# Kernel tuning notes

Measured on AMD Instinct MI355X. Metric: run time of the kernel, lower is better.

Reference implementation:

```python
import jax, jax.numpy as jnp
import numpy as np

KS = 3          # deformable kernel size
PAD = 1         # zero padding
N = KS * KS     # sampling points per pixel
INC = 64
OUTC = 64


def _conv(x, w, stride, pad, groups):
    return jax.lax.conv_general_dilated(
        x, w, (stride, stride), ((pad, pad), (pad, pad)),
        feature_group_count=groups,
        dimension_numbers=('NCHW', 'OIHW', 'NCHW'))


def setup_inputs() -> dict:
    key = jax.random.key(0)
    k = jax.random.split(key, 5)
    b, h, w = 4, 128, 128
    x = jax.random.normal(k[0], (b, INC, h, w), jnp.float32)
    # SeparableConv2d params (bias=False throughout in source)
    p_dw = jax.random.normal(k[1], (INC, 1, 3, 3), jnp.float32) * 0.1     # p_conv depthwise 3x3 pad1
    p_pw = jax.random.normal(k[2], (2 * N, INC, 1, 1), jnp.float32) * 0.1  # p_conv pointwise -> 2N offsets
    c_dw = jax.random.normal(k[3], (INC, 1, KS, KS), jnp.float32) * 0.1    # conv depthwise k=ks stride=ks
    c_pw = jax.random.normal(k[4], (OUTC, INC, 1, 1), jnp.float32) * 0.1   # conv pointwise
    return {'x': x, 'p_dw': p_dw, 'p_pw': p_pw, 'c_dw': c_dw, 'c_pw': c_pw}


def reference(x, p_dw, p_pw, c_dw, c_pw):
    b, c, h, w = x.shape
    offset = _conv(_conv(x, p_dw, 1, 1, INC), p_pw, 1, 0, 1)   # [b, 2N, h, w]
    xp = jnp.pad(x, ((0, 0), (0, 0), (PAD, PAD), (PAD, PAD)))  # zero_padding
    Hp, Wp = h + 2 * PAD, w + 2 * PAD
    # p_n: kernel-relative offsets (row-major over ks x ks, 'ij' meshgrid)
    r = jnp.arange(-(KS - 1) // 2, (KS - 1) // 2 + 1, dtype=jnp.float32)
    pnx, pny = jnp.meshgrid(r, r, indexing='ij')
    p_n = jnp.concatenate([pnx.ravel(), pny.ravel()])[None, :, None, None]  # [1, 2N, 1, 1]
    # p_0: base grid, 1-indexed (accounts for padding), stride=1
    gx = jnp.arange(1, h + 1, dtype=jnp.float32)[None, None, :, None]
    gy = jnp.arange(1, w + 1, dtype=jnp.float32)[None, None, None, :]
    p0 = jnp.concatenate([jnp.broadcast_to(gx, (1, N, h, w)),
                          jnp.broadcast_to(gy, (1, N, h, w))], axis=1)      # [1, 2N, h, w]
    p = (p0 + p_n + offset).transpose(0, 2, 3, 1)                           # [b, h, w, 2N]
    px, py = p[..., :N], p[..., N:]
    fx, fy = jnp.floor(px), jnp.floor(py)
    ltx = jnp.clip(fx, 0, Hp - 1); lty = jnp.clip(fy, 0, Wp - 1)
    rbx = jnp.clip(fx + 1, 0, Hp - 1); rby = jnp.clip(fy + 1, 0, Wp - 1)
    pxc = jnp.clip(px, 0, Hp - 1); pyc = jnp.clip(py, 0, Wp - 1)
    # bilinear weights
    g_lt = (1 + (ltx - pxc)) * (1 + (lty - pyc))
    g_rb = (1 - (rbx - pxc)) * (1 - (rby - pyc))
    g_lb = (1 + (ltx - pxc)) * (1 - (rby - pyc))
    g_rt = (1 - (rbx - pxc)) * (1 + (lty - pyc))
    x_flat = xp.reshape(b, c, Hp * Wp)

    def gather(qx, qy):  # -> [b, c, h, w, N]
        idx = (qx * Wp + qy).astype(jnp.int32).reshape(b, 1, h * w * N)
        return jnp.take_along_axis(x_flat, idx, axis=2).reshape(b, c, h, w, N)

    x_off = (g_lt[:, None] * gather(ltx, lty) + g_rb[:, None] * gather(rbx, rby)
             + g_lb[:, None] * gather(ltx, rby) + g_rt[:, None] * gather(rbx, lty))
    # _reshape_x_offset: [b,c,h,w,N] -> [b,c,h*ks,w*ks]
    x_off = x_off.reshape(b, c, h, w, KS, KS).transpose(0, 1, 2, 4, 3, 5).reshape(b, c, h * KS, w * KS)
    # SeparableConv2d(inc, outc, k=ks, stride=ks)
    return _conv(_conv(x_off, c_dw, KS, 0, INC), c_pw, 1, 0, 1)
```

## Files before the change

kernel.cpp:

```cpp
#include <hip/hip_runtime.h>
#include <hip/hip_fp16.h>

#define Hdim 128
#define Wdim 128
#define Cdim 64
#define HW   (Hdim * Wdim)
#define NPIX (4 * HW)
#define NBLK (NPIX / 64)
#define NXCD 8
#define Hp 130
#define HWp (Hp * Hp)

typedef _Float16 v8h __attribute__((ext_vector_type(8)));
typedef float    v4f __attribute__((ext_vector_type(4)));

__device__ __forceinline__ int xcd_swizzle(int bid, int nblk) {
    return (bid % NXCD) * (nblk / NXCD) + bid / NXCD;
}

__global__ __launch_bounds__(512) void transpose_kernel(
    const float* __restrict__ x,
    __half* __restrict__ xt)
{
    __shared__ float tile[64][65];
    int lane = threadIdx.x & 63;
    int g    = threadIdx.x >> 6;
    int blk  = xcd_swizzle(blockIdx.x, NBLK);
    int pix0 = blk * 64;
    int b    = pix0 >> 14;
    int hw0  = pix0 & (HW - 1);
    int h    = hw0 >> 7;
    int w0   = hw0 & 127;

    {
        int gid = blockIdx.x * 512 + threadIdx.x;
        if (gid < 2064 * 8) {
            int rp  = gid >> 3, sub = gid & 7;
            int img = rp / 516, pos = rp - img * 516;
            int i, j;
            if (pos < 130)      { i = 0;   j = pos; }
            else if (pos < 260) { i = 129; j = pos - 130; }
            else { int p2 = pos - 260; i = 1 + (p2 >> 1); j = (p2 & 1) ? 129 : 0; }
            float4* dst = (float4*)(xt + ((size_t)img * HWp + i * Hp + j) * Cdim);
            dst[sub] = make_float4(0.f, 0.f, 0.f, 0.f);
        }
    }

#pragma unroll
    for (int i = 0; i < 8; ++i) {
        int c = g * 8 + i;
        tile[c][lane] = x[(size_t)(b * Cdim + c) * HW + hw0 + lane];
    }
    __syncthreads();
#pragma unroll
    for (int i = 0; i < 8; ++i) {
        int p = g * 8 + i;
        size_t ppos = ((size_t)b * HWp + (h + 1) * Hp + (w0 + 1 + p)) * Cdim + lane;
        xt[ppos] = (__half)tile[lane][p];
    }
}

__global__ __launch_bounds__(512) void fused_kernel(
    const float* __restrict__ x,
    const float* __restrict__ p_dw,
    const float* __restrict__ p_pw,
    const __half* __restrict__ xt,
    const float* __restrict__ c_dw,
    const float* __restrict__ c_pw,
    float* __restrict__ out)
{
    __shared__ __align__(16) unsigned char smem[26880];
    __shared__ __align__(16) unsigned int geoL[8][320];

    auto part_h = (_Float16 (*)[18][64])smem;
    auto accs_h = (_Float16 (*)[72])smem;
    auto outD   = (float (*)[69])(smem + 9216);

    int lane = threadIdx.x & 63;
    int g    = threadIdx.x >> 6;
    int blk  = xcd_swizzle(blockIdx.x, NBLK);
    int pix0 = blk * 64;
    int pix  = pix0 + lane;
    int w = pix & (Wdim - 1);
    int h = (pix >> 7) & (Hdim - 1);
    int b = pix >> 14;

    int   off9[9];
    float msk9[9];
#pragma unroll
    for (int dh = -1; dh <= 1; ++dh) {
#pragma unroll
        for (int dw = -1; dw <= 1; ++dw) {
            int tap = (dh + 1) * 3 + (dw + 1);
            int hh = h + dh, ww = w + dw;
            bool ok = (hh >= 0) & (hh < Hdim) & (ww >= 0) & (ww < Wdim);
            off9[tap] = ok ? hh * Wdim + ww : 0;
            msk9[tap] = ok ? 1.f : 0.f;
        }
    }

    float t[8];
#pragma unroll
    for (int i = 0; i < 8; ++i) {
        int c = g * 8 + i;
        const float* xb0 = x + (size_t)(b * Cdim + c) * HW;
        float s = 0.f;
#pragma unroll
        for (int tap = 0; tap < 9; ++tap) {
            float v = xb0[off9[tap]] * msk9[tap];
            s += v * p_dw[c * 9 + tap];
        }
        t[i] = s;
    }

#pragma unroll
    for (int j = 0; j < 18; ++j) {
        float s = 0.f;
#pragma unroll
        for (int i = 0; i < 8; ++i)
            s += p_pw[j * Cdim + g * 8 + i] * t[i];
        part_h[g][j][lane] = (_Float16)s;
    }
    __syncthreads();

#pragma unroll
    for (int it = 0; it < 3; ++it) {
        int idx = threadIdx.x + it * 512;
        if (idx < 18 * 64) {
            int j = idx >> 6;
            int p = idx & 63;
            float s = 0.f;
#pragma unroll
            for (int q = 0; q < 8; ++q) s += (float)part_h[q][j][p];
            part_h[0][j][p] = (_Float16)s;
        }
    }
    __syncthreads();

#pragma unroll
    for (int it = 0; it < 2; ++it) {
        int idx = threadIdx.x + it * 512;
        if (idx < 9 * 64) {
            int k = idx >> 6;
            int p = idx & 63;
            int ppix = pix0 + p;
            int pw2 = ppix & (Wdim - 1);
            int ph2 = (ppix >> 7) & (Hdim - 1);

            float px = (float)(ph2 + 1) + (float)(k / 3 - 1) + (float)part_h[0][k][p];
            float py = (float)(pw2 + 1) + (float)(k % 3 - 1) + (float)part_h[0][k + 9][p];

            float fx = floorf(px), fy = floorf(py);
            float ltx = fminf(fmaxf(fx, 0.f), 129.f);
            float lty = fminf(fmaxf(fy, 0.f), 129.f);
            float rbx = fminf(fmaxf(fx + 1.f, 0.f), 129.f);
            float rby = fminf(fmaxf(fy + 1.f, 0.f), 129.f);
            float pxc = fminf(fmaxf(px, 0.f), 129.f);
            float pyc = fminf(fmaxf(py, 0.f), 129.f);

            float glt = (1.f + ltx - pxc) * (1.f + lty - pyc);
            float grb = (1.f - rbx + pxc) * (1.f - rby + pyc);
            float glb = (1.f + ltx - pxc) * (1.f - rby + pyc);
            float grt = (1.f - rbx + pxc) * (1.f + lty - pyc);

            int ix0 = (int)ltx, iy0 = (int)lty, ix1 = (int)rbx, iy1 = (int)rby;

            int base1, base2;
            if (iy1 == iy0 + 1) {
                base1 = ix0 * Hp + iy0;
                base2 = ix1 * Hp + iy0;
            } else {
                glt = glb = grt = grb = 0.f;
                base1 = base2 = 0;
            }

            __half2 wlo = __floats2half2_rn(glt, grt);
            __half2 whi = __floats2half2_rn(glb, grb);
            uint4 pk;
            pk.x = *(const unsigned int*)&wlo;
            pk.y = *(const unsigned int*)&whi;
            pk.z = (unsigned int)base1;
            pk.w = (unsigned int)base2;
            *(uint4*)&geoL[p >> 3][(k * 8 + (p & 7)) * 4] = pk;
        }
    }
    __syncthreads();

    int c2   = lane & 31;
    bool lo  = lane < 32;
    int gu   = __builtin_amdgcn_readfirstlane(g);
    const __half* xb = xt + (size_t)b * HWp * Cdim;

    int gv0, gv1, gv2, gv3, gv4;
    {
        const unsigned int* gb = &geoL[gu][0] + lane;
        gv0 = gb[0];   gv1 = gb[64];  gv2 = gb[128];
        gv3 = gb[192]; gv4 = gb[256];
    }
    float wkx9[9], wky9[9];
#pragma unroll
    for (int k = 0; k < 9; ++k) {
        wkx9[k] = c_dw[(2 * c2) * 9 + k];
        wky9[k] = c_dw[(2 * c2 + 1) * 9 + k];
    }

#define GV(r) ((r)==0?gv0:(r)==1?gv1:(r)==2?gv2:(r)==3?gv3:gv4)
#define RL(f) __builtin_amdgcn_readlane(GV((f) >> 6), (f) & 63)

    float2 acc2[8];
#pragma unroll
    for (int i = 0; i < 8; ++i) acc2[i] = make_float2(0.f, 0.f);

#pragma unroll
    for (int k = 0; k < 9; ++k) {
#pragma unroll
        for (int i = 0; i < 8; ++i) {
            const int f = (k * 8 + i) * 4;
            unsigned int d0 = (unsigned int)RL(f + 0);
            unsigned int d1 = (unsigned int)RL(f + 1);
            int bs1 = RL(f + 2);
            int bs2 = RL(f + 3);
            const unsigned int* p1 = (const unsigned int*)(xb + ((size_t)bs1 << 6));
            const unsigned int* p2 = (const unsigned int*)(xb + ((size_t)bs2 << 6));
            unsigned int v1 = p1[lane];
            unsigned int v2 = p2[lane];
            unsigned int wsu = lo ? d0 : d1;
            __half2 w12 = *(const __half2*)&wsu;
            __half2 v1h = *(const __half2*)&v1;
            __half2 v2h = *(const __half2*)&v2;
            __half2 tt = __hadd2(__hmul2(v1h, __half2half2(__low2half(w12))),
                                 __hmul2(v2h, __half2half2(__high2half(w12))));
            float2 tf = __half22float2(tt);
            acc2[i].x += wkx9[k] * tf.x;
            acc2[i].y += wky9[k] * tf.y;
        }
    }
#undef RL
#undef GV

#pragma unroll
    for (int i = 0; i < 8; ++i) {
        acc2[i].x += __shfl_xor(acc2[i].x, 32);
        acc2[i].y += __shfl_xor(acc2[i].y, 32);
    }
    if (lo) {
#pragma unroll
        for (int i = 0; i < 8; ++i) {
            __half2 hv = __floats2half2_rn(acc2[i].x, acc2[i].y);
            *(__half2*)&accs_h[gu * 8 + i][2 * c2] = hv;
        }
    }
    __syncthreads();

    {
        int pb = gu & 3;
        int ob = gu >> 2;
        int lr = lane & 15;
        int lg = lane >> 4;

        const v8h a0 = *(const v8h*)&accs_h[pb * 16 + lr][lg * 8];
        const v8h a1 = *(const v8h*)&accs_h[pb * 16 + lr][32 + lg * 8];

        v4f d0 = {0.f, 0.f, 0.f, 0.f}, d1 = {0.f, 0.f, 0.f, 0.f};
#pragma unroll
        for (int t2 = 0; t2 < 2; ++t2) {
            int oc = ob * 32 + t2 * 16 + lr;
            const float* wr = c_pw + oc * Cdim + lg * 8;
            v8h b0, b1;
#pragma unroll
            for (int j = 0; j < 8; ++j) {
                b0[j] = (_Float16)wr[j];
                b1[j] = (_Float16)wr[32 + j];
            }
            if (t2 == 0) {
                d0 = __builtin_amdgcn_mfma_f32_16x16x32_f16(a0, b0, d0, 0, 0, 0);
                d0 = __builtin_amdgcn_mfma_f32_16x16x32_f16(a1, b1, d0, 0, 0, 0);
            } else {
                d1 = __builtin_amdgcn_mfma_f32_16x16x32_f16(a0, b0, d1, 0, 0, 0);
                d1 = __builtin_amdgcn_mfma_f32_16x16x32_f16(a1, b1, d1, 0, 0, 0);
            }
        }

#pragma unroll
        for (int r = 0; r < 4; ++r) {
            outD[pb * 16 + lg * 4 + r][ob * 32 + lr]      = d0[r];
            outD[pb * 16 + lg * 4 + r][ob * 32 + 16 + lr] = d1[r];
        }
    }
    __syncthreads();

    int hw = pix & (HW - 1);
    size_t obase = (size_t)b * Cdim * HW + hw;
#pragma unroll
    for (int i = 0; i < 8; ++i)
        out[obase + (size_t)(gu * 8 + i) * HW] = outD[lane][gu * 8 + i];
}

extern "C" void kernel_launch(void* const* d_in, const int* in_sizes, int n_in,
                              void* d_out, int out_size, void* d_ws, size_t ws_size,
                              hipStream_t stream) {
    const float* x    = (const float*)d_in[0];
    const float* p_dw = (const float*)d_in[1];
    const float* p_pw = (const float*)d_in[2];
    const float* c_dw = (const float*)d_in[3];
    const float* c_pw = (const float*)d_in[4];
    float* out = (float*)d_out;

    __half* xt = (__half*)d_ws;

    transpose_kernel<<<dim3(NBLK), dim3(512), 0, stream>>>(x, xt);
    fused_kernel<<<dim3(NBLK), dim3(512), 0, stream>>>(x, p_dw, p_pw, xt, c_dw, c_pw, out);
}
```

Baseline: 54.52 us.

## Fuse offset partial reduction into geometry pass and accumulate gather in half2

Removes the separate reduction pass over the per-group offset partials and its barrier by summing the eight partials directly where sampling geometry is computed. Precomputes byte offsets (base shifted by 7) so the gather loop does a single add instead of a shift and multiply. Keeps the depthwise weights and accumulators as packed half2 and uses hfma2, replacing the float converts and scalar FMAs. The shuffle reduction is done on packed half2. Accumulating nine taps in fp16 risks extra rounding error compared with the fp32 accumulation it replaces.

```diff
diff --git a/kernel.cpp b/kernel.cpp
--- a/kernel.cpp
+++ b/kernel.cpp
@@ -124,31 +124,25 @@
     __syncthreads();
 
 #pragma unroll
-    for (int it = 0; it < 3; ++it) {
-        int idx = threadIdx.x + it * 512;
-        if (idx < 18 * 64) {
-            int j = idx >> 6;
-            int p = idx & 63;
-            float s = 0.f;
-#pragma unroll
-            for (int q = 0; q < 8; ++q) s += (float)part_h[q][j][p];
-            part_h[0][j][p] = (_Float16)s;
-        }
-    }
-    __syncthreads();
-
-#pragma unroll
     for (int it = 0; it < 2; ++it) {
         int idx = threadIdx.x + it * 512;
         if (idx < 9 * 64) {
             int k = idx >> 6;
             int p = idx & 63;
+
+            float offx = 0.f, offy = 0.f;
+#pragma unroll
+            for (int q = 0; q < 8; ++q) {
+                offx += (float)part_h[q][k][p];
+                offy += (float)part_h[q][k + 9][p];
+            }
+
             int ppix = pix0 + p;
             int pw2 = ppix & (Wdim - 1);
             int ph2 = (ppix >> 7) & (Hdim - 1);
 
-            float px = (float)(ph2 + 1) + (float)(k / 3 - 1) + (float)part_h[0][k][p];
-            float py = (float)(pw2 + 1) + (float)(k % 3 - 1) + (float)part_h[0][k + 9][p];
+            float px = (float)(ph2 + 1) + (float)(k / 3 - 1) + offx;
+            float py = (float)(pw2 + 1) + (float)(k % 3 - 1) + offy;
 
             float fx = floorf(px), fy = floorf(py);
             float ltx = fminf(fmaxf(fx, 0.f), 129.f);
@@ -165,13 +159,13 @@
 
             int ix0 = (int)ltx, iy0 = (int)lty, ix1 = (int)rbx, iy1 = (int)rby;
 
-            int base1, base2;
+            unsigned int bb1, bb2;
             if (iy1 == iy0 + 1) {
-                base1 = ix0 * Hp + iy0;
-                base2 = ix1 * Hp + iy0;
+                bb1 = (unsigned int)(ix0 * Hp + iy0) << 7;
+                bb2 = (unsigned int)(ix1 * Hp + iy0) << 7;
             } else {
                 glt = glb = grt = grb = 0.f;
-                base1 = base2 = 0;
+                bb1 = bb2 = 0;
             }
 
             __half2 wlo = __floats2half2_rn(glt, grt);
@@ -179,8 +173,8 @@
             uint4 pk;
             pk.x = *(const unsigned int*)&wlo;
             pk.y = *(const unsigned int*)&whi;
-            pk.z = (unsigned int)base1;
-            pk.w = (unsigned int)base2;
+            pk.z = bb1;
+            pk.w = bb2;
             *(uint4*)&geoL[p >> 3][(k * 8 + (p & 7)) * 4] = pk;
         }
     }
@@ -189,7 +183,7 @@
     int c2   = lane & 31;
     bool lo  = lane < 32;
     int gu   = __builtin_amdgcn_readfirstlane(g);
-    const __half* xb = xt + (size_t)b * HWp * Cdim;
+    const char* xbB = (const char*)(xt + (size_t)b * HWp * Cdim) + (lane << 2);
 
     int gv0, gv1, gv2, gv3, gv4;
     {
@@ -197,19 +191,18 @@
         gv0 = gb[0];   gv1 = gb[64];  gv2 = gb[128];
         gv3 = gb[192]; gv4 = gb[256];
     }
-    float wkx9[9], wky9[9];
-#pragma unroll
-    for (int k = 0; k < 9; ++k) {
-        wkx9[k] = c_dw[(2 * c2) * 9 + k];
-        wky9[k] = c_dw[(2 * c2 + 1) * 9 + k];
-    }
+    __half2 wk2h[9];
+#pragma unroll
+    for (int k = 0; k < 9; ++k)
+        wk2h[k] = __floats2half2_rn(c_dw[(2 * c2) * 9 + k],
+                                    c_dw[(2 * c2 + 1) * 9 + k]);
 
 #define GV(r) ((r)==0?gv0:(r)==1?gv1:(r)==2?gv2:(r)==3?gv3:gv4)
 #define RL(f) __builtin_amdgcn_readlane(GV((f) >> 6), (f) & 63)
 
-    float2 acc2[8];
-#pragma unroll
-    for (int i = 0; i < 8; ++i) acc2[i] = make_float2(0.f, 0.f);
+    __half2 acch[8];
+#pragma unroll
+    for (int i = 0; i < 8; ++i) acch[i] = __floats2half2_rn(0.f, 0.f);
 
 #pragma unroll
     for (int k = 0; k < 9; ++k) {
@@ -218,21 +211,17 @@
             const int f = (k * 8 + i) * 4;
             unsigned int d0 = (unsigned int)RL(f + 0);
             unsigned int d1 = (unsigned int)RL(f + 1);
-            int bs1 = RL(f + 2);
-            int bs2 = RL(f + 3);
-            const unsigned int* p1 = (const unsigned int*)(xb + ((size_t)bs1 << 6));
-            const unsigned int* p2 = (const unsigned int*)(xb + ((size_t)bs2 << 6));
-            unsigned int v1 = p1[lane];
-            unsigned int v2 = p2[lane];
+            unsigned int bb1 = (unsigned int)RL(f + 2);
+            unsigned int bb2 = (unsigned int)RL(f + 3);
+            unsigned int v1 = *(const unsigned int*)(xbB + bb1);
+            unsigned int v2 = *(const unsigned int*)(xbB + bb2);
             unsigned int wsu = lo ? d0 : d1;
             __half2 w12 = *(const __half2*)&wsu;
             __half2 v1h = *(const __half2*)&v1;
             __half2 v2h = *(const __half2*)&v2;
-            __half2 tt = __hadd2(__hmul2(v1h, __half2half2(__low2half(w12))),
-                                 __hmul2(v2h, __half2half2(__high2half(w12))));
-            float2 tf = __half22float2(tt);
-            acc2[i].x += wkx9[k] * tf.x;
-            acc2[i].y += wky9[k] * tf.y;
+            __half2 tt = __hfma2(v2h, __half2half2(__high2half(w12)),
+                                 __hmul2(v1h, __half2half2(__low2half(w12))));
+            acch[i] = __hfma2(wk2h[k], tt, acch[i]);
         }
     }
 #undef RL
@@ -240,15 +229,14 @@
 
 #pragma unroll
     for (int i = 0; i < 8; ++i) {
-        acc2[i].x += __shfl_xor(acc2[i].x, 32);
-        acc2[i].y += __shfl_xor(acc2[i].y, 32);
+        int me = *(int*)&acch[i];
+        int ot = __shfl_xor(me, 32);
+        acch[i] = __hadd2(acch[i], *(__half2*)&ot);
     }
     if (lo) {
 #pragma unroll
-        for (int i = 0; i < 8; ++i) {
-            __half2 hv = __floats2half2_rn(acc2[i].x, acc2[i].y);
-            *(__half2*)&accs_h[gu * 8 + i][2 * c2] = hv;
-        }
+        for (int i = 0; i < 8; ++i)
+            *(__half2*)&accs_h[gu * 8 + i][2 * c2] = acch[i];
     }
     __syncthreads();
 
```

Result: faster. 50.88 us (-6.7%).
